# Kernel optimization log

Measured on AMD Instinct MI355X. Metric: run time of the kernel, lower is better.

The kernel has to match this reference:

```python
import jax, jax.numpy as jnp
import numpy as np

B, H, O, E, CMAP = 8192, 1024, 256, 16, 1000


def setup_inputs() -> dict:
    key = jax.random.key(0)
    k_x, k_w, k_b, k_num, k_c = jax.random.split(key, 5)
    x = jax.random.normal(k_x, (B, H), dtype=jnp.float32)
    num = jax.random.randint(k_num, (B,), 0, CMAP, dtype=jnp.int64)
    c = jax.random.randint(k_c, (CMAP,), 0, E, dtype=jnp.int64)
    # per-expert Linear params (torch default: uniform(-1/sqrt(H), 1/sqrt(H)))
    bound = 1.0 / np.sqrt(H)
    W = jax.random.uniform(k_w, (E, O, H), dtype=jnp.float32, minval=-bound, maxval=bound)
    b = jax.random.uniform(k_b, (E, O), dtype=jnp.float32, minval=-bound, maxval=bound)
    return {"x": x, "W": W, "b": b, "num": num, "c": c}


def reference(x, W, b, num, c):
    # expert id for each sample: layers[c[num[i]]]
    expert = c[num]  # [B]
    # compute all experts' linear outputs in one batched GEMM, then select.
    # logits: [B, E, O]
    logits = jnp.einsum('bh,eoh->beo', x, W) + b[None, :, :]
    sel = jnp.take_along_axis(logits, expert[:, None, None], axis=1)[:, 0, :]  # [B, O]
    return jax.nn.sigmoid(sel)
```

## Files before the change

kernel.cpp:

```cpp
#include <hip/hip_runtime.h>
#include <hip/hip_bf16.h>
#include <stdint.h>

#define B_N   8192
#define H_K   1024
#define O_N   256
#define E_N   16

#define TILE_M    32
#define TILE_N    128
#define BK        64
#define NITER     (H_K / BK)
#define MTILES    24

typedef __attribute__((ext_vector_type(8))) short  short8;
typedef __attribute__((ext_vector_type(4))) float  float4v;
typedef __attribute__((ext_vector_type(4))) int    int4v;

__device__ __forceinline__ short f32_to_bf16(float f) {
    uint32_t u = __builtin_bit_cast(uint32_t, f);
    u += 0x7fffu + ((u >> 16) & 1u);
    return (short)(u >> 16);
}

__device__ __forceinline__ short8 cvt8(float4v v0, float4v v1) {
    short8 s;
    s[0] = f32_to_bf16(v0[0]); s[1] = f32_to_bf16(v0[1]);
    s[2] = f32_to_bf16(v0[2]); s[3] = f32_to_bf16(v0[3]);
    s[4] = f32_to_bf16(v1[0]); s[5] = f32_to_bf16(v1[1]);
    s[6] = f32_to_bf16(v1[2]); s[7] = f32_to_bf16(v1[3]);
    return s;
}

__device__ __forceinline__ float4v mfma16(short8 a, short8 b, float4v c) {
    return __builtin_amdgcn_mfma_f32_16x16x32_bf16(a, b, c, 0, 0, 0);
}

__global__ __launch_bounds__(256, 4) void
k_moe(const float* __restrict__ x, const float* __restrict__ W,
      const float* __restrict__ bias, const int* __restrict__ num,
      const int* __restrict__ c, float* __restrict__ out) {
    const int e   = blockIdx.x;
    const int m0  = blockIdx.y * TILE_M;
    const int n0  = blockIdx.z * TILE_N;
    const int tid = threadIdx.x;

    __shared__ short smem[2 * TILE_M * BK + 2 * TILE_N * BK];
    short (*xs)[TILE_M][BK]  = (short (*)[TILE_M][BK])smem;
    short (*wsh)[TILE_N][BK] = (short (*)[TILE_N][BK])(smem + 2 * TILE_M * BK);
    int* rows = (int*)smem;
    int* wsum = (int*)smem + TILE_M;

    if (tid < TILE_M) rows[tid] = -1;
    __syncthreads();

    unsigned mask = 0;
    {
        const int4v* np = (const int4v*)num;
#pragma unroll
        for (int u = 0; u < 8; ++u) {
            const int4v n4 = np[u * 256 + tid];
#pragma unroll
            for (int j = 0; j < 4; ++j)
                mask |= (unsigned)(c[n4[j]] == e) << (u * 4 + j);
        }
    }
    const int cnt  = __popc(mask);
    const int lane = tid & 63, wv = tid >> 6;
    int incl = cnt;
#pragma unroll
    for (int d = 1; d < 64; d <<= 1) {
        int v = __shfl_up(incl, d, 64);
        if (lane >= d) incl += v;
    }
    if (lane == 63) wsum[wv] = incl;
    __syncthreads();
    int base = 0, total = 0;
#pragma unroll
    for (int w = 0; w < 4; ++w) {
        const int s = wsum[w];
        if (w < wv) base += s;
        total += s;
    }
    int pos = base + incl - cnt;
    if (pos < m0 + TILE_M && pos + cnt > m0) {
#pragma unroll
        for (int u = 0; u < 32; ++u)
            if ((mask >> u) & 1u) {
                const int p = pos++;
                if (p >= m0 && p < m0 + TILE_M)
                    rows[p - m0] = (u >> 2) * 1024 + tid * 4 + (u & 3);
            }
    }
    __syncthreads();

    const int count = total;
    const int g8 = tid >> 3, c8 = tid & 7;
    const int xrow = rows[g8];
    const int wave = tid >> 6;
    const int wm = wave >> 1, wn = wave & 1;
    const int quad = lane >> 4, l16 = lane & 15;
    int rid[4];
#pragma unroll
    for (int r = 0; r < 4; ++r) rid[r] = rows[wm * 16 + quad * 4 + r];
    __syncthreads();

    if (m0 >= count) return;

    const int xphys = (c8 ^ (g8 & 7)) * 8;
    const float* Wbase = W + ((size_t)e * O_N + n0) * H_K;

    float4v xv0, xv1;
    float4v wvv[4][2];

    auto load_x = [&](int k0) {
        if (xrow >= 0) {
            const float4v* p = (const float4v*)(x + (size_t)xrow * H_K + k0 + c8 * 8);
            xv0 = p[0]; xv1 = p[1];
        } else { xv0 = (float4v)0.0f; xv1 = (float4v)0.0f; }
    };
    auto load_w = [&](int k0) {
#pragma unroll
        for (int u = 0; u < 4; ++u) {
            const float4v* p = (const float4v*)(Wbase + (size_t)(u * 32 + g8) * H_K + k0 + c8 * 8);
            wvv[u][0] = p[0]; wvv[u][1] = p[1];
        }
    };
    auto store_x = [&](int buf) {
        *(short8*)&xs[buf][g8][xphys] = cvt8(xv0, xv1);
    };
    auto store_w = [&](int buf) {
#pragma unroll
        for (int u = 0; u < 4; ++u)
            *(short8*)&wsh[buf][u * 32 + g8][xphys] = cvt8(wvv[u][0], wvv[u][1]);
    };

    float4v acc[4];
#pragma unroll
    for (int j = 0; j < 4; ++j) acc[j] = (float4v)0.0f;

    load_x(0); load_w(0);
    store_x(0); store_w(0);

    for (int k = 0; k < NITER; ++k) {
        const int cur = k & 1;
        __syncthreads();
        if (k + 1 < NITER) {
            load_x((k + 1) * BK);
            load_w((k + 1) * BK);
        }

#pragma unroll
        for (int ks = 0; ks < 2; ++ks) {
            const int cx = ((ks * 4 + quad) ^ (l16 & 7)) * 8;
            short8 a  = *(const short8*)&xs[cur][wm * 16 + l16][cx];
            short8 b0 = *(const short8*)&wsh[cur][wn * 64 + l16][cx];
            short8 b1 = *(const short8*)&wsh[cur][wn * 64 + 16 + l16][cx];
            short8 b2 = *(const short8*)&wsh[cur][wn * 64 + 32 + l16][cx];
            short8 b3 = *(const short8*)&wsh[cur][wn * 64 + 48 + l16][cx];
            acc[0] = mfma16(a, b0, acc[0]);
            acc[1] = mfma16(a, b1, acc[1]);
            acc[2] = mfma16(a, b2, acc[2]);
            acc[3] = mfma16(a, b3, acc[3]);
        }

        if (k + 1 < NITER) {
            store_x(1 - cur);
            store_w(1 - cur);
        }
    }

#pragma unroll
    for (int j = 0; j < 4; ++j) {
        const int colg = n0 + wn * 64 + j * 16 + l16;
        const float bv = bias[e * O_N + colg];
#pragma unroll
        for (int r = 0; r < 4; ++r) {
            if (rid[r] >= 0) {
                const float v = acc[j][r] + bv;
                out[(size_t)rid[r] * O_N + colg] = 1.0f / (1.0f + __expf(-v));
            }
        }
    }
}

extern "C" void kernel_launch(void* const* d_in, const int* in_sizes, int n_in,
                              void* d_out, int out_size, void* d_ws, size_t ws_size,
                              hipStream_t stream) {
    const float* x   = (const float*)d_in[0];
    const float* W   = (const float*)d_in[1];
    const float* b   = (const float*)d_in[2];
    const int*   num = (const int*)d_in[3];
    const int*   c   = (const int*)d_in[4];
    float* out = (float*)d_out;
    (void)d_ws; (void)ws_size;

    dim3 gg(E_N, MTILES, O_N / TILE_N);
    k_moe<<<gg, 256, 0, stream>>>(x, W, b, num, c, out);
}
```

Baseline: 115.2 us.

## Keep per-expert weight slice resident in LDS and stream x directly to registers

Restructures the grouped GEMM so each block loads a 64-column by 512-K slice of the expert's weights into LDS once per K-half. It then loops over up to 96 gathered rows split across waves, reading x straight from global memory into registers with a software prefetch ring and converting to bf16 on the fly. The grid changes from (expert, fixed M tiles, N halves) to (expert, 4 N slices, 8 row groups), so each block covers a variable number of 32-row tiles. The intent is to cut repeated weight traffic and LDS staging of x. The cost is one large LDS allocation, lower occupancy, and no overlap between the weight fill and compute.

```diff
diff --git a/kernel.cpp b/kernel.cpp
--- a/kernel.cpp
+++ b/kernel.cpp
@@ -7,11 +7,10 @@
 #define O_N   256
 #define E_N   16
 
-#define TILE_M    32
-#define TILE_N    128
-#define BK        64
-#define NITER     (H_K / BK)
-#define MTILES    24
+#define NSL   4
+#define MG    8
+#define KPH   512
+#define KS_PH 16
 
 typedef __attribute__((ext_vector_type(8))) short  short8;
 typedef __attribute__((ext_vector_type(4))) float  float4v;
@@ -36,22 +35,20 @@
     return __builtin_amdgcn_mfma_f32_16x16x32_bf16(a, b, c, 0, 0, 0);
 }
 
-__global__ __launch_bounds__(256, 4) void
+__global__ __launch_bounds__(256, 2) void
 k_moe(const float* __restrict__ x, const float* __restrict__ W,
       const float* __restrict__ bias, const int* __restrict__ num,
       const int* __restrict__ c, float* __restrict__ out) {
     const int e   = blockIdx.x;
-    const int m0  = blockIdx.y * TILE_M;
-    const int n0  = blockIdx.z * TILE_N;
+    const int n0  = blockIdx.y * 64;
+    const int g   = blockIdx.z;
     const int tid = threadIdx.x;
 
-    __shared__ short smem[2 * TILE_M * BK + 2 * TILE_N * BK];
-    short (*xs)[TILE_M][BK]  = (short (*)[TILE_M][BK])smem;
-    short (*wsh)[TILE_N][BK] = (short (*)[TILE_N][BK])(smem + 2 * TILE_M * BK);
-    int* rows = (int*)smem;
-    int* wsum = (int*)smem + TILE_M;
-
-    if (tid < TILE_M) rows[tid] = -1;
+    __shared__ short wlds[64 * KPH];
+    int* rows_ov = (int*)wlds;
+    int* wsum    = (int*)wlds + 96;
+
+    if (tid < 96) rows_ov[tid] = -1;
     __syncthreads();
 
     unsigned mask = 0;
@@ -66,119 +63,142 @@
         }
     }
     const int cnt  = __popc(mask);
-    const int lane = tid & 63, wv = tid >> 6;
+    const int lane = tid & 63, wave = tid >> 6;
     int incl = cnt;
 #pragma unroll
     for (int d = 1; d < 64; d <<= 1) {
         int v = __shfl_up(incl, d, 64);
         if (lane >= d) incl += v;
     }
-    if (lane == 63) wsum[wv] = incl;
-    __syncthreads();
-    int base = 0, total = 0;
+    if (lane == 63) wsum[wave] = incl;
+    __syncthreads();
+    int base = 0, count = 0;
 #pragma unroll
     for (int w = 0; w < 4; ++w) {
         const int s = wsum[w];
-        if (w < wv) base += s;
-        total += s;
-    }
+        if (w < wave) base += s;
+        count += s;
+    }
+    const int T     = (count + 31) >> 5;
+    const int TG    = (T + MG - 1) / MG;
+    const int TGlim = min(TG, T - g * TG);
+    const int wlo   = g * TG * 32;
+
     int pos = base + incl - cnt;
-    if (pos < m0 + TILE_M && pos + cnt > m0) {
+    if (pos < wlo + 96 && pos + cnt > wlo) {
 #pragma unroll
         for (int u = 0; u < 32; ++u)
             if ((mask >> u) & 1u) {
                 const int p = pos++;
-                if (p >= m0 && p < m0 + TILE_M)
-                    rows[p - m0] = (u >> 2) * 1024 + tid * 4 + (u & 3);
-            }
-    }
-    __syncthreads();
-
-    const int count = total;
-    const int g8 = tid >> 3, c8 = tid & 7;
-    const int xrow = rows[g8];
-    const int wave = tid >> 6;
-    const int wm = wave >> 1, wn = wave & 1;
+                if (p >= wlo && p < wlo + 96)
+                    rows_ov[p - wlo] = (u >> 2) * 1024 + tid * 4 + (u & 3);
+            }
+    }
+    __syncthreads();
+
     const int quad = lane >> 4, l16 = lane & 15;
-    int rid[4];
-#pragma unroll
-    for (int r = 0; r < 4; ++r) rid[r] = rows[wm * 16 + quad * 4 + r];
-    __syncthreads();
-
-    if (m0 >= count) return;
-
-    const int xphys = (c8 ^ (g8 & 7)) * 8;
-    const float* Wbase = W + ((size_t)e * O_N + n0) * H_K;
-
-    float4v xv0, xv1;
-    float4v wvv[4][2];
-
-    auto load_x = [&](int k0) {
-        if (xrow >= 0) {
-            const float4v* p = (const float4v*)(x + (size_t)xrow * H_K + k0 + c8 * 8);
-            xv0 = p[0]; xv1 = p[1];
-        } else { xv0 = (float4v)0.0f; xv1 = (float4v)0.0f; }
-    };
-    auto load_w = [&](int k0) {
-#pragma unroll
-        for (int u = 0; u < 4; ++u) {
-            const float4v* p = (const float4v*)(Wbase + (size_t)(u * 32 + g8) * H_K + k0 + c8 * 8);
-            wvv[u][0] = p[0]; wvv[u][1] = p[1];
-        }
-    };
-    auto store_x = [&](int buf) {
-        *(short8*)&xs[buf][g8][xphys] = cvt8(xv0, xv1);
-    };
-    auto store_w = [&](int buf) {
-#pragma unroll
-        for (int u = 0; u < 4; ++u)
-            *(short8*)&wsh[buf][u * 32 + g8][xphys] = cvt8(wvv[u][0], wvv[u][1]);
-    };
-
-    float4v acc[4];
-#pragma unroll
-    for (int j = 0; j < 4; ++j) acc[j] = (float4v)0.0f;
-
-    load_x(0); load_w(0);
-    store_x(0); store_w(0);
-
-    for (int k = 0; k < NITER; ++k) {
-        const int cur = k & 1;
+    const int lt0 = wave >> 1;
+    const int h   = wave & 1;
+    const int m   = l16 & 7;
+
+    int   ra[2][2];
+    int4v erid[2][2];
+#pragma unroll
+    for (int t = 0; t < 2; ++t) {
+        const int lt = lt0 + 2 * t;
+        const int ok = (lt < TGlim);
+        const int o_ = ok ? lt * 32 : 0;
+        ra[t][0] = ok ? rows_ov[o_ + l16] : -1;
+        ra[t][1] = ok ? rows_ov[o_ + 16 + l16] : -1;
+#pragma unroll
+        for (int mb = 0; mb < 2; ++mb)
+            erid[t][mb] = ok ? *(const int4v*)&rows_ov[o_ + mb * 16 + quad * 4]
+                             : (int4v)(-1);
+    }
+    __syncthreads();
+
+    if (TGlim <= 0) return;
+
+    const int NT = (TGlim > lt0) + (TGlim > lt0 + 2);
+
+    float4v acc[2][2][2];
+#pragma unroll
+    for (int t = 0; t < 2; ++t)
+#pragma unroll
+        for (int i = 0; i < 2; ++i)
+#pragma unroll
+            for (int j = 0; j < 2; ++j) acc[t][i][j] = (float4v)0.0f;
+
+    const int brow0 = (h * 32 + l16) * 64;
+    const int brow1 = (h * 32 + 16 + l16) * 64;
+
+#pragma unroll
+    for (int p = 0; p < 2; ++p) {
+#pragma unroll
+        for (int i = 0; i < 16; ++i) {
+            const int t_ = tid + i * 256;
+            const int r  = t_ >> 6;
+            const int gr = t_ & 63;
+            const float4v* src =
+                (const float4v*)(W + ((size_t)(e * O_N + n0 + r)) * H_K + p * KPH + gr * 8);
+            *(short8*)&wlds[(r * 64 + (gr ^ (r & 7))) * 8] = cvt8(src[0], src[1]);
+        }
         __syncthreads();
-        if (k + 1 < NITER) {
-            load_x((k + 1) * BK);
-            load_w((k + 1) * BK);
-        }
-
-#pragma unroll
-        for (int ks = 0; ks < 2; ++ks) {
-            const int cx = ((ks * 4 + quad) ^ (l16 & 7)) * 8;
-            short8 a  = *(const short8*)&xs[cur][wm * 16 + l16][cx];
-            short8 b0 = *(const short8*)&wsh[cur][wn * 64 + l16][cx];
-            short8 b1 = *(const short8*)&wsh[cur][wn * 64 + 16 + l16][cx];
-            short8 b2 = *(const short8*)&wsh[cur][wn * 64 + 32 + l16][cx];
-            short8 b3 = *(const short8*)&wsh[cur][wn * 64 + 48 + l16][cx];
-            acc[0] = mfma16(a, b0, acc[0]);
-            acc[1] = mfma16(a, b1, acc[1]);
-            acc[2] = mfma16(a, b2, acc[2]);
-            acc[3] = mfma16(a, b3, acc[3]);
-        }
-
-        if (k + 1 < NITER) {
-            store_x(1 - cur);
-            store_w(1 - cur);
-        }
-    }
-
-#pragma unroll
-    for (int j = 0; j < 4; ++j) {
-        const int colg = n0 + wn * 64 + j * 16 + l16;
-        const float bv = bias[e * O_N + colg];
-#pragma unroll
-        for (int r = 0; r < 4; ++r) {
-            if (rid[r] >= 0) {
-                const float v = acc[j][r] + bv;
-                out[(size_t)rid[r] * O_N + colg] = 1.0f / (1.0f + __expf(-v));
+
+        for (int t = 0; t < NT; ++t) {
+            const int r0 = (ra[t][0] < 0) ? 0 : ra[t][0];
+            const int r1 = (ra[t][1] < 0) ? 0 : ra[t][1];
+            const float* xb0 = x + (size_t)r0 * H_K + p * KPH + quad * 8;
+            const float* xb1 = x + (size_t)r1 * H_K + p * KPH + quad * 8;
+
+            float4v xbuf[4][4];
+#pragma unroll
+            for (int s = 0; s < 4; ++s) {
+                xbuf[s][0] = *(const float4v*)(xb0 + s * 32);
+                xbuf[s][1] = *(const float4v*)(xb0 + s * 32 + 4);
+                xbuf[s][2] = *(const float4v*)(xb1 + s * 32);
+                xbuf[s][3] = *(const float4v*)(xb1 + s * 32 + 4);
+            }
+#pragma unroll
+            for (int ks = 0; ks < KS_PH; ++ks) {
+                const int s = ks & 3;
+                const short8 a0 = cvt8(xbuf[s][0], xbuf[s][1]);
+                const short8 a1 = cvt8(xbuf[s][2], xbuf[s][3]);
+                const int gph = ((ks * 4 + quad) ^ m);
+                const short8 b0 = *(const short8*)&wlds[(brow0 + gph) * 8];
+                const short8 b1 = *(const short8*)&wlds[(brow1 + gph) * 8];
+                acc[t][0][0] = mfma16(a0, b0, acc[t][0][0]);
+                acc[t][0][1] = mfma16(a0, b1, acc[t][0][1]);
+                acc[t][1][0] = mfma16(a1, b0, acc[t][1][0]);
+                acc[t][1][1] = mfma16(a1, b1, acc[t][1][1]);
+                if (ks + 4 < KS_PH) {
+                    xbuf[s][0] = *(const float4v*)(xb0 + (ks + 4) * 32);
+                    xbuf[s][1] = *(const float4v*)(xb0 + (ks + 4) * 32 + 4);
+                    xbuf[s][2] = *(const float4v*)(xb1 + (ks + 4) * 32);
+                    xbuf[s][3] = *(const float4v*)(xb1 + (ks + 4) * 32 + 4);
+                }
+            }
+        }
+        if (p == 0) __syncthreads();
+    }
+
+#pragma unroll
+    for (int t = 0; t < 2; ++t) {
+        if (t >= NT) break;
+#pragma unroll
+        for (int nf = 0; nf < 2; ++nf) {
+            const int colg = n0 + h * 32 + nf * 16 + l16;
+            const float bv = bias[e * O_N + colg];
+#pragma unroll
+            for (int mb = 0; mb < 2; ++mb) {
+#pragma unroll
+                for (int j = 0; j < 4; ++j) {
+                    const int rid = erid[t][mb][j];
+                    if (rid >= 0) {
+                        const float v = acc[t][mb][nf][j] + bv;
+                        out[(size_t)rid * O_N + colg] = 1.0f / (1.0f + __expf(-v));
+                    }
+                }
             }
         }
     }
@@ -195,6 +215,6 @@
     float* out = (float*)d_out;
     (void)d_ws; (void)ws_size;
 
-    dim3 gg(E_N, MTILES, O_N / TILE_N);
+    dim3 gg(E_N, NSL, MG);
     k_moe<<<gg, 256, 0, stream>>>(x, W, b, num, c, out);
 }
```

Result: slower. 154.9 us (+34.5%).

## Split K across two wave groups with 64-row tiles and direct-register A operands

Applied to the files above, without the earlier changes.

Doubles the M tile to 64 rows and launches 512-thread blocks, with two wave groups each handling half of the K dimension. The partial sums are reduced through shared memory before the sigmoid epilogue. The x operand is loaded straight from global memory into registers and converted to bf16 in place, no longer staged through LDS. Each wave now covers all 128 output columns, so one A fragment feeds eight MFMAs. The aim is more reuse of each W tile and fewer LDS round trips, at the cost of a larger shared footprint (64KB) and an extra reduction step.

```diff
diff --git a/kernel.cpp b/kernel.cpp
--- a/kernel.cpp
+++ b/kernel.cpp
@@ -7,11 +7,11 @@
 #define O_N   256
 #define E_N   16
 
-#define TILE_M    32
-#define TILE_N    128
-#define BK        64
-#define NITER     (H_K / BK)
-#define MTILES    24
+#define TILE_M  64
+#define TILE_N  128
+#define BK      64
+#define NITER   8
+#define MTILES  12
 
 typedef __attribute__((ext_vector_type(8))) short  short8;
 typedef __attribute__((ext_vector_type(4))) float  float4v;
@@ -36,7 +36,7 @@
     return __builtin_amdgcn_mfma_f32_16x16x32_bf16(a, b, c, 0, 0, 0);
 }
 
-__global__ __launch_bounds__(256, 4) void
+__global__ __launch_bounds__(512, 4) void
 k_moe(const float* __restrict__ x, const float* __restrict__ W,
       const float* __restrict__ bias, const int* __restrict__ num,
       const int* __restrict__ c, float* __restrict__ out) {
@@ -45,21 +45,19 @@
     const int n0  = blockIdx.z * TILE_N;
     const int tid = threadIdx.x;
 
-    __shared__ short smem[2 * TILE_M * BK + 2 * TILE_N * BK];
-    short (*xs)[TILE_M][BK]  = (short (*)[TILE_M][BK])smem;
-    short (*wsh)[TILE_N][BK] = (short (*)[TILE_N][BK])(smem + 2 * TILE_M * BK);
-    int* rows = (int*)smem;
-    int* wsum = (int*)smem + TILE_M;
-
-    if (tid < TILE_M) rows[tid] = -1;
+    __shared__ short S[32768];
+    int* rows_ov = (int*)S;
+    int* wsum    = (int*)S + 64;
+
+    if (tid < TILE_M) rows_ov[tid] = -1;
     __syncthreads();
 
     unsigned mask = 0;
     {
         const int4v* np = (const int4v*)num;
 #pragma unroll
-        for (int u = 0; u < 8; ++u) {
-            const int4v n4 = np[u * 256 + tid];
+        for (int u = 0; u < 4; ++u) {
+            const int4v n4 = np[u * 512 + tid];
 #pragma unroll
             for (int j = 0; j < 4; ++j)
                 mask |= (unsigned)(c[n4[j]] == e) << (u * 4 + j);
@@ -75,110 +73,125 @@
     }
     if (lane == 63) wsum[wv] = incl;
     __syncthreads();
-    int base = 0, total = 0;
-#pragma unroll
-    for (int w = 0; w < 4; ++w) {
+    int base = 0, count = 0;
+#pragma unroll
+    for (int w = 0; w < 8; ++w) {
         const int s = wsum[w];
         if (w < wv) base += s;
-        total += s;
+        count += s;
     }
     int pos = base + incl - cnt;
     if (pos < m0 + TILE_M && pos + cnt > m0) {
 #pragma unroll
-        for (int u = 0; u < 32; ++u)
-            if ((mask >> u) & 1u) {
+        for (int b = 0; b < 16; ++b)
+            if ((mask >> b) & 1u) {
                 const int p = pos++;
                 if (p >= m0 && p < m0 + TILE_M)
-                    rows[p - m0] = (u >> 2) * 1024 + tid * 4 + (u & 3);
+                    rows_ov[p - m0] = (b >> 2) * 2048 + tid * 4 + (b & 3);
             }
     }
     __syncthreads();
 
-    const int count = total;
-    const int g8 = tid >> 3, c8 = tid & 7;
-    const int xrow = rows[g8];
-    const int wave = tid >> 6;
-    const int wm = wave >> 1, wn = wave & 1;
     const int quad = lane >> 4, l16 = lane & 15;
-    int rid[4];
-#pragma unroll
-    for (int r = 0; r < 4; ++r) rid[r] = rows[wm * 16 + quad * 4 + r];
+    const int grp  = wv >> 2;
+    const int wl   = wv & 3;
+    const int ra_  = rows_ov[wl * 16 + l16];
+    const int rax  = (ra_ < 0) ? 0 : ra_;
+    const int4v erid = *(const int4v*)&rows_ov[wl * 16 + quad * 4];
     __syncthreads();
 
     if (m0 >= count) return;
 
-    const int xphys = (c8 ^ (g8 & 7)) * 8;
-    const float* Wbase = W + ((size_t)e * O_N + n0) * H_K;
-
-    float4v xv0, xv1;
-    float4v wvv[4][2];
-
-    auto load_x = [&](int k0) {
-        if (xrow >= 0) {
-            const float4v* p = (const float4v*)(x + (size_t)xrow * H_K + k0 + c8 * 8);
-            xv0 = p[0]; xv1 = p[1];
-        } else { xv0 = (float4v)0.0f; xv1 = (float4v)0.0f; }
+    const float* xp = x + (size_t)rax * H_K + grp * 512 + quad * 8;
+
+    float4v wv4[4][2];
+    float4v av[2][2][2];
+
+    auto ldW = [&](int i) {
+#pragma unroll
+        for (int u = 0; u < 4; ++u) {
+            const int gid = u * 512 + tid;
+            const int gg  = gid >> 10;
+            const int row = (gid >> 3) & 127;
+            const int cw  = gid & 7;
+            const float4v* src = (const float4v*)(W + ((size_t)(e * O_N + n0 + row)) * H_K
+                                                    + gg * 512 + i * BK + cw * 8);
+            wv4[u][0] = src[0]; wv4[u][1] = src[1];
+        }
     };
-    auto load_w = [&](int k0) {
+    auto stW = [&](int buf) {
 #pragma unroll
         for (int u = 0; u < 4; ++u) {
-            const float4v* p = (const float4v*)(Wbase + (size_t)(u * 32 + g8) * H_K + k0 + c8 * 8);
-            wvv[u][0] = p[0]; wvv[u][1] = p[1];
+            const int gid = u * 512 + tid;
+            const int gg  = gid >> 10;
+            const int row = (gid >> 3) & 127;
+            const int cw  = gid & 7;
+            *(short8*)&S[buf * 16384 + gg * 8192 + row * 64 + ((cw ^ (row & 7)) * 8)]
+                = cvt8(wv4[u][0], wv4[u][1]);
         }
     };
-    auto store_x = [&](int buf) {
-        *(short8*)&xs[buf][g8][xphys] = cvt8(xv0, xv1);
+    auto ldA = [&](int buf, int i) {
+#pragma unroll
+        for (int ks = 0; ks < 2; ++ks) {
+            const float4v* p = (const float4v*)(xp + i * BK + ks * 32);
+            av[buf][ks][0] = p[0]; av[buf][ks][1] = p[1];
+        }
     };
-    auto store_w = [&](int buf) {
-#pragma unroll
-        for (int u = 0; u < 4; ++u)
-            *(short8*)&wsh[buf][u * 32 + g8][xphys] = cvt8(wvv[u][0], wvv[u][1]);
-    };
-
-    float4v acc[4];
-#pragma unroll
-    for (int j = 0; j < 4; ++j) acc[j] = (float4v)0.0f;
-
-    load_x(0); load_w(0);
-    store_x(0); store_w(0);
-
-    for (int k = 0; k < NITER; ++k) {
-        const int cur = k & 1;
+
+    float4v acc[8];
+#pragma unroll
+    for (int j = 0; j < 8; ++j) acc[j] = (float4v)0.0f;
+
+    ldW(0); ldA(0, 0);
+    stW(0);
+
+    for (int i = 0; i < NITER; ++i) {
+        const int cur = i & 1;
         __syncthreads();
-        if (k + 1 < NITER) {
-            load_x((k + 1) * BK);
-            load_w((k + 1) * BK);
+        if (i + 1 < NITER) {
+            ldW(i + 1);
+            ldA(1 - cur, i + 1);
         }
 
 #pragma unroll
         for (int ks = 0; ks < 2; ++ks) {
+            const short8 a = cvt8(av[cur][ks][0], av[cur][ks][1]);
             const int cx = ((ks * 4 + quad) ^ (l16 & 7)) * 8;
-            short8 a  = *(const short8*)&xs[cur][wm * 16 + l16][cx];
-            short8 b0 = *(const short8*)&wsh[cur][wn * 64 + l16][cx];
-            short8 b1 = *(const short8*)&wsh[cur][wn * 64 + 16 + l16][cx];
-            short8 b2 = *(const short8*)&wsh[cur][wn * 64 + 32 + l16][cx];
-            short8 b3 = *(const short8*)&wsh[cur][wn * 64 + 48 + l16][cx];
-            acc[0] = mfma16(a, b0, acc[0]);
-            acc[1] = mfma16(a, b1, acc[1]);
-            acc[2] = mfma16(a, b2, acc[2]);
-            acc[3] = mfma16(a, b3, acc[3]);
-        }
-
-        if (k + 1 < NITER) {
-            store_x(1 - cur);
-            store_w(1 - cur);
-        }
-    }
-
-#pragma unroll
-    for (int j = 0; j < 4; ++j) {
-        const int colg = n0 + wn * 64 + j * 16 + l16;
+            const int bb = cur * 16384 + grp * 8192;
+#pragma unroll
+            for (int nb = 0; nb < 8; ++nb) {
+                const short8 b = *(const short8*)&S[bb + (nb * 16 + l16) * 64 + cx];
+                acc[nb] = mfma16(a, b, acc[nb]);
+            }
+        }
+
+        if (i + 1 < NITER) stW(1 - cur);
+    }
+
+    __syncthreads();
+    float* red = (float*)S;
+    if (grp == 1) {
+#pragma unroll
+        for (int nb = 0; nb < 8; ++nb)
+#pragma unroll
+            for (int r = 0; r < 4; ++r)
+                red[wl * 2112 + (quad * 4 + r) * 132 + nb * 16 + l16] = acc[nb][r];
+    }
+    __syncthreads();
+    if (grp == 1) return;
+
+#pragma unroll
+    for (int nb = 0; nb < 8; ++nb) {
+        const int colg = n0 + nb * 16 + l16;
         const float bv = bias[e * O_N + colg];
 #pragma unroll
         for (int r = 0; r < 4; ++r) {
-            if (rid[r] >= 0) {
-                const float v = acc[j][r] + bv;
-                out[(size_t)rid[r] * O_N + colg] = 1.0f / (1.0f + __expf(-v));
+            const int p = m0 + wl * 16 + quad * 4 + r;
+            if (p < count) {
+                const float v = acc[nb][r]
+                              + red[wl * 2112 + (quad * 4 + r) * 132 + nb * 16 + l16]
+                              + bv;
+                out[(size_t)erid[r] * O_N + colg] = 1.0f / (1.0f + __expf(-v));
             }
         }
     }
@@ -196,5 +209,5 @@
     (void)d_ws; (void)ws_size;
 
     dim3 gg(E_N, MTILES, O_N / TILE_N);
-    k_moe<<<gg, 256, 0, stream>>>(x, W, b, num, c, out);
-}
+    k_moe<<<gg, 512, 0, stream>>>(x, W, b, num, c, out);
+}
```

After: 119.9 us. +4.1%, slower.
